# Kernel optimization log

Hardware: AMD Instinct MI355X
Metric: run time of the kernel (lower is better)

Reference implementation:

```python
import jax, jax.numpy as jnp
import numpy as np

D = 128  # node_state_dim
T = 8    # message-passing steps
FEAT = 26


def _dense_relu(x, W, b):
    return jax.nn.relu(x @ W + b)


def _gru(x, h, k, rk, bi, br):
    # Keras GRUCell (reset_after=True) math, inference (no dropout).
    xz, xr, xh = jnp.split(x @ k + bi, 3, axis=-1)
    hz, hr, hh = jnp.split(h @ rk + br, 3, axis=-1)
    z = jax.nn.sigmoid(xz + hz)
    r = jax.nn.sigmoid(xr + hr)
    hcand = jnp.tanh(xh + r * hh)
    return z * h + (1.0 - z) * hcand


def _segment_mean(data, ids, num_segments):
    s = jax.ops.segment_sum(data, ids, num_segments=num_segments)
    cnt = jax.ops.segment_sum(jnp.ones((data.shape[0],), data.dtype), ids,
                              num_segments=num_segments)
    return jnp.where(cnt[:, None] > 0, s / jnp.maximum(cnt, 1.0)[:, None], 0.0)


def setup_inputs() -> dict:
    key = jax.random.key(0)
    ks = jax.random.split(key, 24)
    n_i, n_c, n_e = 50000, 100000, 200000
    glorot = lambda k, shape: jax.random.normal(k, shape, jnp.float32) * np.sqrt(2.0 / (shape[0] + shape[1]))
    inp = {
        'feature_connection': jax.random.normal(ks[0], (n_c, FEAT), jnp.float32),
        'src_ip_to_connection': jax.random.randint(ks[1], (n_e,), 0, n_i),
        'dst_ip_to_connection': jax.random.randint(ks[2], (n_e,), 0, n_c),
        'src_connection_to_ip': jax.random.randint(ks[3], (n_e,), 0, n_c),
        'dst_connection_to_ip': jax.random.randint(ks[4], (n_e,), 0, n_i),
        'n_i': n_i, 'n_c': n_c,
        # message MLPs: Dense(2D -> D)
        'Wm1': glorot(ks[5], (2 * D, D)), 'bm1': jnp.zeros((D,), jnp.float32),
        'Wm2': glorot(ks[6], (2 * D, D)), 'bm2': jnp.zeros((D,), jnp.float32),
        # GRU cells: kernel [D,3D], recurrent_kernel [D,3D], input/recurrent biases [3D]
        'k_ip': glorot(ks[7], (D, 3 * D)), 'rk_ip': glorot(ks[8], (D, 3 * D)),
        'bi_ip': jnp.zeros((3 * D,), jnp.float32), 'br_ip': jnp.zeros((3 * D,), jnp.float32),
        'k_conn': glorot(ks[9], (D, 3 * D)), 'rk_conn': glorot(ks[10], (D, 3 * D)),
        'bi_conn': jnp.zeros((3 * D,), jnp.float32), 'br_conn': jnp.zeros((3 * D,), jnp.float32),
        # readout: D -> 128 -> 64 -> 15 softmax
        'Wr1': glorot(ks[11], (D, 128)), 'br1': jnp.zeros((128,), jnp.float32),
        'Wr2': glorot(ks[12], (128, 64)), 'br2': jnp.zeros((64,), jnp.float32),
        'Wr3': glorot(ks[13], (64, 15)), 'br3': jnp.zeros((15,), jnp.float32),
    }
    return inp


def reference(feature_connection, src_ip_to_connection, dst_ip_to_connection,
              src_connection_to_ip, dst_connection_to_ip, n_i, n_c,
              Wm1, bm1, Wm2, bm2,
              k_ip, rk_ip, bi_ip, br_ip,
              k_conn, rk_conn, bi_conn, br_conn,
              Wr1, br1, Wr2, br2, Wr3, br3):
    ip_state = jnp.ones((n_i, D), jnp.float32)
    connection_state = jnp.concatenate(
        [feature_connection, jnp.zeros((n_c, D - FEAT), jnp.float32)], axis=1)

    def step(carry, _):
        ip_state, connection_state = carry
        # ip -> connection messages
        nn_in1 = jnp.concatenate([ip_state[src_ip_to_connection],
                                  connection_state[dst_ip_to_connection]], axis=1)
        ip_message = _dense_relu(nn_in1, Wm1, bm1)
        ip_mean = _segment_mean(ip_message, dst_ip_to_connection, n_c)
        # connection -> ip messages
        nn_in2 = jnp.concatenate([connection_state[src_connection_to_ip],
                                  ip_state[dst_connection_to_ip]], axis=1)
        conn_message = _dense_relu(nn_in2, Wm2, bm2)
        conn_mean = _segment_mean(conn_message, dst_connection_to_ip, n_i)
        ip_state = _gru(conn_mean, ip_state, k_ip, rk_ip, bi_ip, br_ip)
        connection_state = _gru(ip_mean, connection_state, k_conn, rk_conn, bi_conn, br_conn)
        return (ip_state, connection_state), None

    (ip_state, connection_state), _ = jax.lax.scan(step, (ip_state, connection_state),
                                                   None, length=T)
    h = _dense_relu(connection_state, Wr1, br1)
    h = _dense_relu(h, Wr2, br2)
    return jax.nn.softmax(h @ Wr3 + br3, axis=-1)
```

## Files before the change

### kernel.cpp

```cpp
#include <hip/hip_runtime.h>
#include <math.h>

#define D 128
#define T_STEPS 8
#define FEAT 26

typedef short bf16x8 __attribute__((ext_vector_type(8)));
typedef unsigned short u16x8 __attribute__((ext_vector_type(8)));
typedef float f32x4 __attribute__((ext_vector_type(4)));

__device__ inline unsigned short f2bf(float f) {
    unsigned b = __float_as_uint(f);
    b += 0x7FFFu + ((b >> 16) & 1u);
    return (unsigned short)(b >> 16);
}
__device__ inline float bf2f(unsigned short u) {
    return __uint_as_float(((unsigned)u) << 16);
}

__device__ inline void gl_lds16(const void* g, void* l) {
    __builtin_amdgcn_global_load_lds(
        (const __attribute__((address_space(1))) void*)g,
        (__attribute__((address_space(3))) void*)l, 16, 0, 0);
}

__device__ inline float fast_sigmoid(float x) {
    float e = __builtin_amdgcn_exp2f(-1.442695041f * x);
    return __builtin_amdgcn_rcpf(1.0f + e);
}
__device__ inline float fast_tanh(float x) {
    float e = __builtin_amdgcn_exp2f(2.885390082f * x);
    return 1.0f - 2.0f * __builtin_amdgcn_rcpf(1.0f + e);
}

__global__ void k_init_dual(unsigned short* __restrict__ ip_state,
                            unsigned short* __restrict__ conn_state,
                            const float* __restrict__ feat, int ni_elems,
                            int total) {
    int i = blockIdx.x * blockDim.x + threadIdx.x;
    if (i < ni_elems) {
        ip_state[i] = 0x3F80;
    } else if (i < total) {
        int j = i - ni_elems;
        int r = j >> 7, d = j & 127;
        conn_state[j] = (d < FEAT) ? f2bf(feat[r * FEAT + d]) : (unsigned short)0;
    }
}

__global__ void k_gbias_dual(const float* __restrict__ bi0, const float* __restrict__ br0,
                             float* __restrict__ cb0,
                             const float* __restrict__ bi1, const float* __restrict__ br1,
                             float* __restrict__ cb1) {
    const float* bi = blockIdx.x ? bi1 : bi0;
    const float* br = blockIdx.x ? br1 : br0;
    float* cb = blockIdx.x ? cb1 : cb0;
    int d = threadIdx.x;
    cb[d] = bi[d] + br[d];
    cb[128 + d] = bi[128 + d] + br[128 + d];
    cb[256 + d] = bi[256 + d];
    cb[384 + d] = br[256 + d];
}

__global__ void k_pack_pq_dual(const float* __restrict__ Wm1,
                               const float* __restrict__ Wm2,
                               short* __restrict__ WGip, short* __restrict__ WGcn) {
    int id = blockIdx.x * blockDim.x + threadIdx.x;
    if (id < 4 * 16 * 512) {
        int i = id & 7;
        int l = (id >> 3) & 63;
        int rest = id >> 9;
        int q = rest % 16;
        int s = rest / 16;
        int k = s * 32 + (l >> 4) * 8 + i;
        int col = q * 16 + (l & 15);
        float fip = (col < 128) ? Wm1[k * 128 + col] : Wm2[(128 + k) * 128 + (col - 128)];
        float fcn = (col < 128) ? Wm2[k * 128 + col] : Wm1[(128 + k) * 128 + (col - 128)];
        WGip[id] = (short)f2bf(fip);
        WGcn[id] = (short)f2bf(fcn);
    }
}

__global__ void k_pack_gru_dual(const float* __restrict__ K0, const float* __restrict__ RK0,
                                short* __restrict__ WG0,
                                const float* __restrict__ K1, const float* __restrict__ RK1,
                                short* __restrict__ WG1, int nblk0) {
    int total = 8 * 24 * 512;
    bool sec = blockIdx.x >= nblk0;
    const float* K = sec ? K1 : K0;
    const float* RK = sec ? RK1 : RK0;
    short* WG = sec ? WG1 : WG0;
    int id = (sec ? blockIdx.x - nblk0 : blockIdx.x) * blockDim.x + threadIdx.x;
    if (id < total) {
        int i = id & 7;
        int l = (id >> 3) & 63;
        int rest = id >> 9;
        int q = rest % 24;
        int s = rest / 24;
        int ct = (s < 4) ? q : (q < 16 ? q : q + 8);
        int k = s * 32 + (l >> 4) * 8 + i;
        int col = ct * 16 + (l & 15);
        float v = 0.f;
        if (k < 128) {
            if (col < 384) v = K[k * 384 + col];
        } else {
            int kk = k - 128;
            if (col < 256) v = RK[kk * 384 + col];
            else if (col >= 384) v = RK[kk * 384 + (col - 128)];
        }
        WG[id] = (short)f2bf(v);
    }
}

__global__ void k_pack_r1(const float* __restrict__ Wf, short* __restrict__ WG) {
    int id = blockIdx.x * blockDim.x + threadIdx.x;
    if (id < 4 * 8 * 512) {
        int i = id & 7;
        int l = (id >> 3) & 63;
        int rest = id >> 9;
        int q = rest % 8;
        int s = rest / 8;
        int k = s * 32 + (l >> 4) * 8 + i;
        int col = q * 16 + (l & 15);
        WG[id] = (short)f2bf(Wf[(size_t)k * 128 + col]);
    }
}

__global__ void k_counts(const int* __restrict__ dst_a, const int* __restrict__ dst_b,
                         int* __restrict__ cnt_c, int* __restrict__ cnt_i, int n_e) {
    int i = blockIdx.x * blockDim.x + threadIdx.x;
    if (i < n_e) {
        atomicAdd(&cnt_c[dst_a[i]], 1);
        atomicAdd(&cnt_i[dst_b[i]], 1);
    }
}

__device__ inline void scan1_body(const int* cnt, int* off, int* bsum, int n, int blk) {
    __shared__ int wsh[4];
    int tid = threadIdx.x, lane = tid & 63, wid = tid >> 6;
    int base = blk * 2048 + tid * 8;
    int v[8], pref[8];
    int s = 0;
#pragma unroll
    for (int j = 0; j < 8; ++j) {
        v[j] = (base + j < n) ? cnt[base + j] : 0;
        pref[j] = s; s += v[j];
    }
    int x = s;
#pragma unroll
    for (int o = 1; o < 64; o <<= 1) {
        int y = __shfl_up(x, o, 64);
        if (lane >= o) x += y;
    }
    if (lane == 63) wsh[wid] = x;
    __syncthreads();
    int wbase = 0, tot = 0;
#pragma unroll
    for (int w = 0; w < 4; ++w) { if (w < wid) wbase += wsh[w]; tot += wsh[w]; }
    int tbase = wbase + (x - s);
#pragma unroll
    for (int j = 0; j < 8; ++j)
        if (base + j < n) off[base + j] = tbase + pref[j];
    if (tid == 0) bsum[blk] = tot;
}

__global__ void k_scan1_dual(const int* __restrict__ cnt_c, int* __restrict__ off_c,
                             int* __restrict__ bsum_c, int n_c, int nb_c,
                             const int* __restrict__ cnt_i, int* __restrict__ off_i,
                             int* __restrict__ bsum_i, int n_i) {
    if ((int)blockIdx.x < nb_c) scan1_body(cnt_c, off_c, bsum_c, n_c, blockIdx.x);
    else scan1_body(cnt_i, off_i, bsum_i, n_i, blockIdx.x - nb_c);
}

__global__ void k_scan2_dual(int* __restrict__ bsum_c, int nb_c,
                             int* __restrict__ bsum_i, int nb_i) {
    __shared__ int wsh[4];
    int* bsum = blockIdx.x ? bsum_i : bsum_c;
    int nb = blockIdx.x ? nb_i : nb_c;
    int tid = threadIdx.x, lane = tid & 63, wid = tid >> 6;
    int v = (tid < nb) ? bsum[tid] : 0;
    int x = v;
#pragma unroll
    for (int o = 1; o < 64; o <<= 1) {
        int y = __shfl_up(x, o, 64);
        if (lane >= o) x += y;
    }
    if (lane == 63) wsh[wid] = x;
    __syncthreads();
    int wbase = 0;
#pragma unroll
    for (int w = 0; w < 4; ++w) if (w < wid) wbase += wsh[w];
    if (tid < nb) bsum[tid] = wbase + (x - v);
}

__global__ void k_scan3_dual(int* __restrict__ off_c, const int* __restrict__ bsum_c,
                             int n_c,
                             int* __restrict__ off_i, const int* __restrict__ bsum_i,
                             int n_i) {
    int i = blockIdx.x * blockDim.x + threadIdx.x;
    if (i < n_c) off_c[i] += bsum_c[i >> 11];
    else if (i < n_c + n_i) {
        int j = i - n_c;
        off_i[j] += bsum_i[j >> 11];
    }
}

__global__ void k_scatter_dual(
    const int* __restrict__ dst0, const int* __restrict__ src0,
    const int* __restrict__ off0, int* __restrict__ cur0, int* __restrict__ el0,
    const int* __restrict__ dst1, const int* __restrict__ src1,
    const int* __restrict__ off1, int* __restrict__ cur1, int* __restrict__ el1,
    int n_e, int nb_e) {
    bool sec = (int)blockIdx.x >= nb_e;
    const int* dst = sec ? dst1 : dst0;
    const int* src = sec ? src1 : src0;
    const int* off = sec ? off1 : off0;
    int* cursor = sec ? cur1 : cur0;
    int* elist = sec ? el1 : el0;
    int i = (sec ? blockIdx.x - nb_e : blockIdx.x) * blockDim.x + threadIdx.x;
    if (i < n_e) {
        int d = dst[i];
        int pos = off[d] + atomicAdd(&cursor[d], 1);
        elist[pos] = src[i];
    }
}

template <int KSTEPS, int NCT, int EPI, int OUTBF>
__global__ __launch_bounds__(256, 4) void k_mgemm9_dual(
    const unsigned short* __restrict__ S0, const unsigned short* __restrict__ S1,
    int sstride,
    const short* __restrict__ WG0, const short* __restrict__ WG1,
    const float* __restrict__ bias,
    void* __restrict__ O0, void* __restrict__ O1, int ostride,
    int nblk0, int n0, int n1)
{
    constexpr int NQW = NCT / 2;
    constexpr int PHU = NCT * 64;
    __shared__ short lw[2][PHU * 8];
    int b = blockIdx.x;
    bool sec = b >= nblk0;
    const unsigned short* S = sec ? S1 : S0;
    const short* WG = sec ? WG1 : WG0;
    void* OUT = sec ? O1 : O0;
    int n = sec ? n1 : n0;
    int r0 = (sec ? b - nblk0 : b) * 64;

    int tid = threadIdx.x;
    int l = tid & 63, w = tid >> 6;
    int rt = w >> 1, cg = w & 1;
    int g = l >> 4, ln = l & 15;
    int rb = r0 + rt * 32;
    int rowc0 = rb + ln;      if (rowc0 >= n) rowc0 = n - 1;
    int rowc1 = rb + 16 + ln; if (rowc1 >= n) rowc1 = n - 1;

#pragma unroll
    for (int t = 0; t < PHU / 256; ++t)
        gl_lds16(WG + ((size_t)(t * 256 + tid)) * 8,
                 &lw[0][(size_t)(t * 256 + w * 64) * 8]);

    bf16x8 u0[KSTEPS], u1[KSTEPS];
#pragma unroll
    for (int s = 0; s < KSTEPS; ++s) {
        u0[s] = *(const bf16x8*)&S[(size_t)rowc0 * sstride + s * 32 + g * 8];
        u1[s] = *(const bf16x8*)&S[(size_t)rowc1 * sstride + s * 32 + g * 8];
    }

    f32x4 acc0[NQW], acc1[NQW];
#pragma unroll
    for (int c = 0; c < NQW; ++c) {
        acc0[c] = (f32x4){0.f, 0.f, 0.f, 0.f};
        acc1[c] = (f32x4){0.f, 0.f, 0.f, 0.f};
    }
    __syncthreads();

#pragma unroll
    for (int s = 0; s < KSTEPS; ++s) {
        if (s + 1 < KSTEPS) {
#pragma unroll
            for (int t = 0; t < PHU / 256; ++t)
                gl_lds16(WG + ((size_t)(s + 1) * PHU + t * 256 + tid) * 8,
                         &lw[(s + 1) & 1][(size_t)(t * 256 + w * 64) * 8]);
        }
        const short* lb = lw[s & 1];
#pragma unroll
        for (int c = 0; c < NQW; ++c) {
            int q = cg * NQW + c;
            bf16x8 wv = *(const bf16x8*)&lb[((size_t)q * 64 + l) * 8];
            acc0[c] = __builtin_amdgcn_mfma_f32_16x16x32_bf16(u0[s], wv, acc0[c], 0, 0, 0);
            acc1[c] = __builtin_amdgcn_mfma_f32_16x16x32_bf16(u1[s], wv, acc1[c], 0, 0, 0);
        }
        __syncthreads();
    }

#pragma unroll
    for (int c = 0; c < NQW; ++c) {
        int col = (cg * NQW + c) * 16 + ln;
        float bv = (EPI == 1) ? bias[col] : 0.f;
#pragma unroll
        for (int i = 0; i < 4; ++i) {
            int gr0 = rb + g * 4 + i;
            int gr1 = gr0 + 16;
            float v0 = acc0[c][i], v1 = acc1[c][i];
            if (EPI == 1) { v0 = fmaxf(v0 + bv, 0.f); v1 = fmaxf(v1 + bv, 0.f); }
            if (OUTBF == 1) {
                unsigned short* O = (unsigned short*)OUT;
                if (gr0 < n) O[(size_t)gr0 * ostride + col] = f2bf(v0);
                if (gr1 < n) O[(size_t)gr1 * ostride + col] = f2bf(v1);
            } else {
                float* O = (float*)OUT;
                if (gr0 < n) O[(size_t)gr0 * ostride + col] = v0;
                if (gr1 < n) O[(size_t)gr1 * ostride + col] = v1;
            }
        }
    }
}

__global__ __launch_bounds__(256, 2) void k_gru11_dual(
    const unsigned short* __restrict__ P0, const unsigned short* __restrict__ Q0,
    const int* __restrict__ el0, const int* __restrict__ of0,
    const int* __restrict__ ct0, const float* __restrict__ mb0,
    unsigned short* __restrict__ H0, const short* __restrict__ WGa,
    const float* __restrict__ cba,
    const unsigned short* __restrict__ P1, const unsigned short* __restrict__ Q1,
    const int* __restrict__ el1, const int* __restrict__ of1,
    const int* __restrict__ ct1, const float* __restrict__ mb1,
    unsigned short* __restrict__ H1, const short* __restrict__ WGb,
    const float* __restrict__ cbb,
    int nblk0, int n0, int n1)
{
    constexpr int PHU1 = 24 * 64;
    __shared__ short lw[2 * PHU1 * 8];
    __shared__ unsigned short xs[64][136];
    int b = blockIdx.x;
    bool sec = b >= nblk0;
    const unsigned short* Pother = sec ? P1 : P0;
    const unsigned short* Qown   = sec ? Q1 : Q0;
    const int* elist = sec ? el1 : el0;
    const int* off   = sec ? of1 : of0;
    const int* cnt   = sec ? ct1 : ct0;
    const float* mb  = sec ? mb1 : mb0;
    unsigned short* state = sec ? H1 : H0;
    const short* WG = sec ? WGb : WGa;
    const float* cb = sec ? cbb : cba;
    int n = sec ? n1 : n0;
    int r0 = (sec ? b - nblk0 : b) * 64;

    int tid = threadIdx.x;
    int l = tid & 63, w = tid >> 6;
    int rt = w >> 1, cg = w & 1;
    int g = l >> 4, ln = l & 15;
    int rb = r0 + rt * 32;

#pragma unroll
    for (int t = 0; t < 12; ++t)
        gl_lds16(WG + ((size_t)(t * 256 + tid)) * 8,
                 &lw[(size_t)(t * 256 + w * 64) * 8]);

    {
        int lr = tid >> 2;
        int cq = (tid & 3) * 32;
        int node = r0 + lr; if (node >= n) node = n - 1;
        int deg = cnt[node];
        float av[32];
#pragma unroll
        for (int k = 0; k < 32; ++k) av[k] = 0.f;
        if (deg > 0) {
            int o = off[node];
            float qvf[32];
#pragma unroll
            for (int jj = 0; jj < 4; ++jj) {
                u16x8 qv8 = *(const u16x8*)&Qown[(size_t)node * 256 + cq + jj * 8];
#pragma unroll
                for (int k = 0; k < 8; ++k)
                    qvf[jj * 8 + k] = bf2f(qv8[k]) + mb[cq + jj * 8 + k];
            }
            for (int e = 0; e < deg; ++e) {
                int sidx = elist[o + e];
                const unsigned short* prow = Pother + (size_t)sidx * 256 + cq;
#pragma unroll
                for (int jj = 0; jj < 4; ++jj) {
                    u16x8 pv = *(const u16x8*)&prow[jj * 8];
#pragma unroll
                    for (int k = 0; k < 8; ++k)
                        av[jj * 8 + k] += fmaxf(bf2f(pv[k]) + qvf[jj * 8 + k], 0.f);
                }
            }
            float inv = 1.0f / (float)deg;
#pragma unroll
            for (int k = 0; k < 32; ++k) av[k] *= inv;
        }
#pragma unroll
        for (int jj = 0; jj < 4; ++jj) {
            u16x8 o8;
#pragma unroll
            for (int k = 0; k < 8; ++k) o8[k] = f2bf(av[jj * 8 + k]);
            *(u16x8*)&xs[lr][cq + jj * 8] = o8;
        }
    }
    __syncthreads();

    int lrow0 = rt * 32 + ln;
    int lrow1 = lrow0 + 16;
    bf16x8 u0[4], u1[4];
#pragma unroll
    for (int ss = 0; ss < 4; ++ss) {
        u0[ss] = *(const bf16x8*)&xs[lrow0][ss * 32 + g * 8];
        u1[ss] = *(const bf16x8*)&xs[lrow1][ss * 32 + g * 8];
    }

    f32x4 acc0[16], acc1[16];
#pragma unroll
    for (int c = 0; c < 16; ++c) {
        acc0[c] = (f32x4){0.f, 0.f, 0.f, 0.f};
        acc1[c] = (f32x4){0.f, 0.f, 0.f, 0.f};
    }

#pragma unroll
    for (int p = 0; p < 4; ++p) {
        if (p > 0) {
#pragma unroll
            for (int t = 0; t < 12; ++t)
                gl_lds16(WG + ((size_t)p * 2 * PHU1 + t * 256 + tid) * 8,
                         &lw[(size_t)(t * 256 + w * 64) * 8]);
            if (p == 2) {
#pragma unroll
                for (int i = 0; i < 4; ++i) {
                    int id = i * 256 + tid;
                    int r = id >> 4, c8 = id & 15;
                    int gr = r0 + r; if (gr >= n) gr = n - 1;
                    *(u16x8*)&xs[r][c8 * 8] =
                        *(const u16x8*)&state[(size_t)gr * 128 + c8 * 8];
                }
            }
            __syncthreads();
            if (p == 2) {
#pragma unroll
                for (int s2 = 0; s2 < 4; ++s2) {
                    u0[s2] = *(const bf16x8*)&xs[lrow0][s2 * 32 + g * 8];
                    u1[s2] = *(const bf16x8*)&xs[lrow1][s2 * 32 + g * 8];
                }
            }
        }
#pragma unroll
        for (int sub = 0; sub < 2; ++sub) {
            const int s = p * 2 + sub;
            const int ss = s & 3;
            const short* lb = lw + (size_t)sub * PHU1 * 8;
#pragma unroll
            for (int jp = 0; jp < 4; ++jp) {
                int qz = cg * 4 + jp;
                int qr = 8 + cg * 4 + jp;
                int qh = 16 + cg * 4 + jp;
                int aih = (s < 4) ? (8 + jp) : (12 + jp);
#define PROC(Q, AI) do {                                                        \
                bf16x8 wv = *(const bf16x8*)&lb[(((size_t)(Q)) * 64 + l) * 8];  \
                acc0[AI] = __builtin_amdgcn_mfma_f32_16x16x32_bf16(u0[ss], wv, acc0[AI], 0, 0, 0); \
                acc1[AI] = __builtin_amdgcn_mfma_f32_16x16x32_bf16(u1[ss], wv, acc1[AI], 0, 0, 0); \
            } while (0)
                PROC(qz, jp);
                PROC(qr, 4 + jp);
                PROC(qh, aih);
#undef PROC
            }
        }
        if (p + 1 < 4) __syncthreads();
    }

#pragma unroll
    for (int jp = 0; jp < 4; ++jp) {
        int d = (cg * 4 + jp) * 16 + ln;
        float bz = cb[d], brr = cb[128 + d], bxh = cb[256 + d], bhh = cb[384 + d];
#pragma unroll
        for (int rs = 0; rs < 2; ++rs) {
            f32x4 az = rs ? acc1[jp] : acc0[jp];
            f32x4 ar = rs ? acc1[4 + jp] : acc0[4 + jp];
            f32x4 axh = rs ? acc1[8 + jp] : acc0[8 + jp];
            f32x4 ahh = rs ? acc1[12 + jp] : acc0[12 + jp];
#pragma unroll
            for (int i = 0; i < 4; ++i) {
                int lr = rt * 32 + rs * 16 + g * 4 + i;
                int gr = r0 + lr;
                if (gr < n) {
                    float h = bf2f(xs[lr][d]);
                    float z = fast_sigmoid(az[i] + bz);
                    float r = fast_sigmoid(ar[i] + brr);
                    float hc = fast_tanh(axh[i] + bxh + r * (ahh[i] + bhh));
                    state[(size_t)gr * 128 + d] = f2bf(z * h + (1.0f - z) * hc);
                }
            }
        }
    }
}

__global__ __launch_bounds__(256) void k_read2(
    const float* __restrict__ h1,
    const float* __restrict__ W2, const float* __restrict__ b2,
    const float* __restrict__ W3, const float* __restrict__ b3,
    float* __restrict__ out, int n)
{
    __shared__ float W2ls[128][64];
    __shared__ float W3ls[64][16];
    __shared__ float h1ls[8][132];
    __shared__ float h2ls[8][66];
    __shared__ float lgls[8][16];
    int tid = threadIdx.x;
    int r0 = blockIdx.x * 8;

#pragma unroll
    for (int i = 0; i < 8; ++i) {
        int id = i * 256 + tid;
        int kr = id >> 4, c4 = id & 15;
        *(float4*)&W2ls[kr][c4 * 4] = *(const float4*)&W2[kr * 64 + c4 * 4];
    }
    for (int id = tid; id < 960; id += 256) {
        W3ls[id / 15][id % 15] = W3[id];
    }
    {
        int r = tid >> 5, c4 = tid & 31;
        int gr = r0 + r; if (gr >= n) gr = n - 1;
        *(float4*)&h1ls[r][c4 * 4] = *(const float4*)&h1[(size_t)gr * 128 + c4 * 4];
    }
    __syncthreads();

    {
        int row = tid >> 5, c = tid & 31;
        float a0 = b2[c], a1 = b2[c + 32];
        for (int k = 0; k < 128; ++k) {
            float h = h1ls[row][k];
            a0 = fmaf(h, W2ls[k][c], a0);
            a1 = fmaf(h, W2ls[k][c + 32], a1);
        }
        h2ls[row][c] = fmaxf(a0, 0.f);
        h2ls[row][c + 32] = fmaxf(a1, 0.f);
    }
    __syncthreads();

    if (tid < 120) {
        int row = tid / 15, c = tid % 15;
        float a = b3[c];
        for (int k = 0; k < 64; ++k) a = fmaf(h2ls[row][k], W3ls[k][c], a);
        lgls[row][c] = a;
    }
    __syncthreads();

    if (tid < 120) {
        int row = tid / 15, c = tid % 15;
        int gr = r0 + row;
        if (gr < n) {
            float m = -1e30f;
#pragma unroll
            for (int k = 0; k < 15; ++k) m = fmaxf(m, lgls[row][k]);
            float s = 0.f;
#pragma unroll
            for (int k = 0; k < 15; ++k) s += expf(lgls[row][k] - m);
            out[(size_t)gr * 15 + c] = expf(lgls[row][c] - m) / s;
        }
    }
}

extern "C" void kernel_launch(void* const* d_in, const int* in_sizes, int n_in,
                              void* d_out, int out_size, void* d_ws, size_t ws_size,
                              hipStream_t stream) {
    const float* feat   = (const float*)d_in[0];
    const int*   src_ip = (const int*)d_in[1];
    const int*   dst_ip = (const int*)d_in[2];
    const int*   src_cn = (const int*)d_in[3];
    const int*   dst_cn = (const int*)d_in[4];
    const float* Wm1 = (const float*)d_in[7];
    const float* bm1 = (const float*)d_in[8];
    const float* Wm2 = (const float*)d_in[9];
    const float* bm2 = (const float*)d_in[10];
    const float* k_ip  = (const float*)d_in[11];
    const float* rk_ip = (const float*)d_in[12];
    const float* bi_ip = (const float*)d_in[13];
    const float* br_ip = (const float*)d_in[14];
    const float* k_cn  = (const float*)d_in[15];
    const float* rk_cn = (const float*)d_in[16];
    const float* bi_cn = (const float*)d_in[17];
    const float* br_cn = (const float*)d_in[18];
    const float* Wr1 = (const float*)d_in[19];
    const float* br1 = (const float*)d_in[20];
    const float* Wr2 = (const float*)d_in[21];
    const float* br2 = (const float*)d_in[22];
    const float* Wr3 = (const float*)d_in[23];
    const float* br3 = (const float*)d_in[24];

    const int n_e = in_sizes[1];
    const int n_c = in_sizes[0] / FEAT;
    const int n_i = 50000;

    auto align = [](size_t x) { return (x + 255) & ~(size_t)255; };
    char* ws = (char*)d_ws;
    size_t off = 0;
    unsigned short* ip_state   = (unsigned short*)(ws + off); off = align(off + (size_t)n_i * D * 2);
    unsigned short* conn_state = (unsigned short*)(ws + off); off = align(off + (size_t)n_c * D * 2);
    unsigned short* PQ_ip = (unsigned short*)(ws + off); off = align(off + (size_t)n_i * 256 * 2);
    unsigned short* PQ_cn = (unsigned short*)(ws + off); off = align(off + (size_t)n_c * 256 * 2);
    float* h1buf      = (float*)(ws + off); off = align(off + (size_t)n_c * 128 * 4);
    short* WGpq_ip    = (short*)(ws + off); off = align(off + (size_t)4 * 16 * 512 * 2);
    short* WGpq_cn    = (short*)(ws + off); off = align(off + (size_t)4 * 16 * 512 * 2);
    short* WGg_ip     = (short*)(ws + off); off = align(off + (size_t)8 * 24 * 512 * 2);
    short* WGg_cn     = (short*)(ws + off); off = align(off + (size_t)8 * 24 * 512 * 2);
    short* WGr1       = (short*)(ws + off); off = align(off + (size_t)4 * 8 * 512 * 2);
    float* cb_ip      = (float*)(ws + off); off = align(off + (size_t)512 * 4);
    float* cb_cn      = (float*)(ws + off); off = align(off + (size_t)512 * 4);
    int*   zb         = (int*)(ws + off);   off = align(off + (size_t)(2 * n_c + 2 * n_i) * 4);
    int*   cnt_c      = zb;
    int*   cnt_i      = zb + n_c;
    int*   cursor_c   = zb + n_c + n_i;
    int*   cursor_i   = zb + 2 * n_c + n_i;
    int*   off_c      = (int*)(ws + off);   off = align(off + (size_t)n_c * 4);
    int*   off_i      = (int*)(ws + off);   off = align(off + (size_t)n_i * 4);
    int*   elist_c    = (int*)(ws + off);   off = align(off + (size_t)n_e * 4);
    int*   elist_i    = (int*)(ws + off);   off = align(off + (size_t)n_e * 4);
    int*   bsum_c     = (int*)(ws + off);   off = align(off + (size_t)64 * 4);
    int*   bsum_i     = (int*)(ws + off);   off = align(off + (size_t)64 * 4);

    int init_total = n_i * D + n_c * D;
    k_init_dual<<<(init_total + 255) / 256, 256, 0, stream>>>(
        ip_state, conn_state, feat, n_i * D, init_total);

    k_pack_pq_dual<<<(4 * 16 * 512 + 255) / 256, 256, 0, stream>>>(
        Wm1, Wm2, WGpq_ip, WGpq_cn);
    {
        int nbg = (8 * 24 * 512 + 255) / 256;
        k_pack_gru_dual<<<2 * nbg, 256, 0, stream>>>(
            k_ip, rk_ip, WGg_ip, k_cn, rk_cn, WGg_cn, nbg);
    }
    k_pack_r1<<<(4 * 8 * 512 + 255) / 256, 256, 0, stream>>>(Wr1, WGr1);
    k_gbias_dual<<<2, 128, 0, stream>>>(bi_ip, br_ip, cb_ip, bi_cn, br_cn, cb_cn);

    hipMemsetAsync(zb, 0, (size_t)(2 * n_c + 2 * n_i) * 4, stream);
    k_counts<<<(n_e + 255) / 256, 256, 0, stream>>>(dst_ip, dst_cn, cnt_c, cnt_i, n_e);
    int nb_c = (n_c + 2047) / 2048, nb_i = (n_i + 2047) / 2048;
    k_scan1_dual<<<nb_c + nb_i, 256, 0, stream>>>(
        cnt_c, off_c, bsum_c, n_c, nb_c, cnt_i, off_i, bsum_i, n_i);
    k_scan2_dual<<<2, 256, 0, stream>>>(bsum_c, nb_c, bsum_i, nb_i);
    k_scan3_dual<<<(n_c + n_i + 255) / 256, 256, 0, stream>>>(
        off_c, bsum_c, n_c, off_i, bsum_i, n_i);
    {
        int nb_e = (n_e + 255) / 256;
        k_scatter_dual<<<2 * nb_e, 256, 0, stream>>>(
            dst_ip, src_ip, off_c, cursor_c, elist_c,
            dst_cn, src_cn, off_i, cursor_i, elist_i, n_e, nb_e);
    }

    int b64_i = (n_i + 63) / 64;
    int b64_c = (n_c + 63) / 64;

    for (int t = 0; t < T_STEPS; ++t) {
        k_mgemm9_dual<4, 16, 0, 1><<<b64_i + b64_c, 256, 0, stream>>>(
            ip_state, conn_state, 128, WGpq_ip, WGpq_cn, nullptr,
            PQ_ip, PQ_cn, 256, b64_i, n_i, n_c);
        k_gru11_dual<<<b64_i + b64_c, 256, 0, stream>>>(
            PQ_cn, PQ_ip + 128, elist_i, off_i, cnt_i, bm2, ip_state, WGg_ip, cb_ip,
            PQ_ip, PQ_cn + 128, elist_c, off_c, cnt_c, bm1, conn_state, WGg_cn, cb_cn,
            b64_i, n_i, n_c);
    }

    k_mgemm9_dual<4, 8, 1, 0><<<b64_c, 256, 0, stream>>>(
        conn_state, conn_state, 128, WGr1, WGr1, br1,
        h1buf, h1buf, 128, b64_c, n_c, n_c);
    k_read2<<<(n_c + 7) / 8, 256, 0, stream>>>(
        h1buf, Wr2, br2, Wr3, br3, (float*)d_out, n_c);
}
```

Before: 1.291 ms.

## Halve GRU kernel weight LDS buffer for higher occupancy and unroll gather by two

The GRU kernel now stages one weight sub-phase (instead of two) in LDS per barrier, halving shared memory so launch bounds can ask for three blocks per CU. The edge-gather loop is unrolled by two so loads from two source rows are in flight together. The trade-off is twice as many barriers and weight-staging rounds, plus more register pressure from the unrolled loads under a tighter register budget.

```diff
diff --git a/kernel.cpp b/kernel.cpp
--- a/kernel.cpp
+++ b/kernel.cpp
@@ -314,7 +314,7 @@
     }
 }
 
-__global__ __launch_bounds__(256, 2) void k_gru11_dual(
+__global__ __launch_bounds__(256, 3) void k_gru12_dual(
     const unsigned short* __restrict__ P0, const unsigned short* __restrict__ Q0,
     const int* __restrict__ el0, const int* __restrict__ of0,
     const int* __restrict__ ct0, const float* __restrict__ mb0,
@@ -328,7 +328,7 @@
     int nblk0, int n0, int n1)
 {
     constexpr int PHU1 = 24 * 64;
-    __shared__ short lw[2 * PHU1 * 8];
+    __shared__ short lw[PHU1 * 8];
     __shared__ unsigned short xs[64][136];
     int b = blockIdx.x;
     bool sec = b >= nblk0;
@@ -351,7 +351,7 @@
     int rb = r0 + rt * 32;
 
 #pragma unroll
-    for (int t = 0; t < 12; ++t)
+    for (int t = 0; t < 6; ++t)
         gl_lds16(WG + ((size_t)(t * 256 + tid)) * 8,
                  &lw[(size_t)(t * 256 + w * 64) * 8]);
 
@@ -373,12 +373,33 @@
                 for (int k = 0; k < 8; ++k)
                     qvf[jj * 8 + k] = bf2f(qv8[k]) + mb[cq + jj * 8 + k];
             }
-            for (int e = 0; e < deg; ++e) {
-                int sidx = elist[o + e];
-                const unsigned short* prow = Pother + (size_t)sidx * 256 + cq;
+            int e = 0;
+            for (; e + 2 <= deg; e += 2) {
+                int s0 = elist[o + e], s1 = elist[o + e + 1];
+                const unsigned short* pr0 = Pother + (size_t)s0 * 256 + cq;
+                const unsigned short* pr1 = Pother + (size_t)s1 * 256 + cq;
+                u16x8 p0[4], p1[4];
+#pragma unroll
+                for (int jj = 0; jj < 4; ++jj) p0[jj] = *(const u16x8*)&pr0[jj * 8];
+#pragma unroll
+                for (int jj = 0; jj < 4; ++jj) p1[jj] = *(const u16x8*)&pr1[jj * 8];
+#pragma unroll
+                for (int jj = 0; jj < 4; ++jj)
+#pragma unroll
+                    for (int k = 0; k < 8; ++k)
+                        av[jj * 8 + k] += fmaxf(bf2f(p0[jj][k]) + qvf[jj * 8 + k], 0.f);
+#pragma unroll
+                for (int jj = 0; jj < 4; ++jj)
+#pragma unroll
+                    for (int k = 0; k < 8; ++k)
+                        av[jj * 8 + k] += fmaxf(bf2f(p1[jj][k]) + qvf[jj * 8 + k], 0.f);
+            }
+            if (e < deg) {
+                int s0 = elist[o + e];
+                const unsigned short* pr0 = Pother + (size_t)s0 * 256 + cq;
 #pragma unroll
                 for (int jj = 0; jj < 4; ++jj) {
-                    u16x8 pv = *(const u16x8*)&prow[jj * 8];
+                    u16x8 pv = *(const u16x8*)&pr0[jj * 8];
 #pragma unroll
                     for (int k = 0; k < 8; ++k)
                         av[jj * 8 + k] += fmaxf(bf2f(pv[k]) + qvf[jj * 8 + k], 0.f);
@@ -415,13 +436,14 @@
     }
 
 #pragma unroll
-    for (int p = 0; p < 4; ++p) {
-        if (p > 0) {
-#pragma unroll
-            for (int t = 0; t < 12; ++t)
-                gl_lds16(WG + ((size_t)p * 2 * PHU1 + t * 256 + tid) * 8,
+    for (int s = 0; s < 8; ++s) {
+        const int ss = s & 3;
+        if (s > 0) {
+#pragma unroll
+            for (int t = 0; t < 6; ++t)
+                gl_lds16(WG + ((size_t)s * PHU1 + t * 256 + tid) * 8,
                          &lw[(size_t)(t * 256 + w * 64) * 8]);
-            if (p == 2) {
+            if (s == 4) {
 #pragma unroll
                 for (int i = 0; i < 4; ++i) {
                     int id = i * 256 + tid;
@@ -432,7 +454,7 @@
                 }
             }
             __syncthreads();
-            if (p == 2) {
+            if (s == 4) {
 #pragma unroll
                 for (int s2 = 0; s2 < 4; ++s2) {
                     u0[s2] = *(const bf16x8*)&xs[lrow0][s2 * 32 + g * 8];
@@ -441,28 +463,22 @@
             }
         }
 #pragma unroll
-        for (int sub = 0; sub < 2; ++sub) {
-            const int s = p * 2 + sub;
-            const int ss = s & 3;
-            const short* lb = lw + (size_t)sub * PHU1 * 8;
-#pragma unroll
-            for (int jp = 0; jp < 4; ++jp) {
-                int qz = cg * 4 + jp;
-                int qr = 8 + cg * 4 + jp;
-                int qh = 16 + cg * 4 + jp;
-                int aih = (s < 4) ? (8 + jp) : (12 + jp);
+        for (int jp = 0; jp < 4; ++jp) {
+            int qz = cg * 4 + jp;
+            int qr = 8 + cg * 4 + jp;
+            int qh = 16 + cg * 4 + jp;
+            int aih = (s < 4) ? (8 + jp) : (12 + jp);
 #define PROC(Q, AI) do {                                                        \
-                bf16x8 wv = *(const bf16x8*)&lb[(((size_t)(Q)) * 64 + l) * 8];  \
-                acc0[AI] = __builtin_amdgcn_mfma_f32_16x16x32_bf16(u0[ss], wv, acc0[AI], 0, 0, 0); \
-                acc1[AI] = __builtin_amdgcn_mfma_f32_16x16x32_bf16(u1[ss], wv, acc1[AI], 0, 0, 0); \
-            } while (0)
-                PROC(qz, jp);
-                PROC(qr, 4 + jp);
-                PROC(qh, aih);
+            bf16x8 wv = *(const bf16x8*)&lw[(((size_t)(Q)) * 64 + l) * 8];      \
+            acc0[AI] = __builtin_amdgcn_mfma_f32_16x16x32_bf16(u0[ss], wv, acc0[AI], 0, 0, 0); \
+            acc1[AI] = __builtin_amdgcn_mfma_f32_16x16x32_bf16(u1[ss], wv, acc1[AI], 0, 0, 0); \
+        } while (0)
+            PROC(qz, jp);
+            PROC(qr, 4 + jp);
+            PROC(qh, aih);
 #undef PROC
-            }
-        }
-        if (p + 1 < 4) __syncthreads();
+        }
+        if (s + 1 < 8) __syncthreads();
     }
 
 #pragma unroll
@@ -651,7 +667,7 @@
         k_mgemm9_dual<4, 16, 0, 1><<<b64_i + b64_c, 256, 0, stream>>>(
             ip_state, conn_state, 128, WGpq_ip, WGpq_cn, nullptr,
             PQ_ip, PQ_cn, 256, b64_i, n_i, n_c);
-        k_gru11_dual<<<b64_i + b64_c, 256, 0, stream>>>(
+        k_gru12_dual<<<b64_i + b64_c, 256, 0, stream>>>(
             PQ_cn, PQ_ip + 128, elist_i, off_i, cnt_i, bm2, ip_state, WGg_ip, cb_ip,
             PQ_ip, PQ_cn + 128, elist_c, off_c, cnt_c, bm1, conn_state, WGg_cn, cb_cn,
             b64_i, n_i, n_c);
```

After: 1.260 ms. -2.4%, faster.
